# Kernel optimization log

Measured on AMD Instinct MI355X. Metric: run time of the kernel, lower is better.

The kernel has to match this reference:

```python
import jax, jax.numpy as jnp
import numpy as np

N_NODES = 30000
N_EDGES = 480000
IN = 64
HID = 32
OUT = 64
H1, H2 = 4, 4


def _xavier(key, shape, gain=1.4142135623730951):
    fan_out, fan_in = shape
    std = gain * (2.0 / (fan_in + fan_out)) ** 0.5
    return std * jax.random.normal(key, shape, dtype=jnp.float32)


def setup_inputs() -> dict:
    key = jax.random.key(0)
    ks = jax.random.split(key, 12)
    nfeats = jax.random.normal(ks[0], (N_NODES, IN), dtype=jnp.float32)
    efeats = jax.random.normal(ks[1], (N_EDGES, IN), dtype=jnp.float32)
    src = jax.random.randint(ks[2], (N_EDGES,), 0, N_NODES, dtype=jnp.int32)
    dst = jax.random.randint(ks[3], (N_EDGES,), 0, N_NODES, dtype=jnp.int32)
    # layer 1 params: in_node=IN, in_edge=IN, out_node=out_edge=HID, heads=H1
    W_nodes1 = _xavier(ks[4], (HID * H1, IN))
    b_nodes1 = jnp.zeros((HID * H1,), dtype=jnp.float32)
    W_edges1 = _xavier(ks[5], (HID * H1, 3 * IN))
    W_attn1 = _xavier(ks[6], (H1, HID))
    # layer 2 params: in_node=in_edge=HID*H1, out_node=out_edge=OUT, heads=H2
    d2 = HID * H1
    W_nodes2 = _xavier(ks[7], (OUT * H2, d2))
    b_nodes2 = jnp.zeros((OUT * H2,), dtype=jnp.float32)
    W_edges2 = _xavier(ks[8], (OUT * H2, 3 * d2))
    W_attn2 = _xavier(ks[9], (H2, OUT))
    return {
        "nfeats": nfeats, "efeats": efeats, "src": src, "dst": dst,
        "W_nodes1": W_nodes1, "b_nodes1": b_nodes1, "W_edges1": W_edges1, "W_attn1": W_attn1,
        "W_nodes2": W_nodes2, "b_nodes2": b_nodes2, "W_edges2": W_edges2, "W_attn2": W_attn2,
    }


def _egat_layer(hn, he, src, dst, Wn, bn, We, Wa, num_heads, out_n, out_e, first_layer, n_nodes):
    # first layer: node 'h' overwritten by sum-aggregation of incoming edge feats
    if first_layer:
        hn = jax.ops.segment_sum(he, dst, num_segments=n_nodes)
    E = he.shape[0]
    # edge attention on raw node feats: [h_src | f | h_dst] -> fc_edges -> leaky_relu
    stack = jnp.concatenate([hn[src], he, hn[dst]], axis=-1)          # [E, 2*dn + de]
    f_out = jax.nn.leaky_relu(stack @ We.T)                            # [E, H*out_e]
    f_out = f_out.reshape(E, num_heads, out_e)                         # new edge feats
    # a = fc_attn(f_out).sum(-1)  ==  f_out . (column-sum of W_attn)
    a = jnp.einsum("ehf,f->eh", f_out, Wa.sum(axis=0))                 # [E, H]
    # projected node feats used as messages
    hp = (hn @ Wn.T + bn).reshape(n_nodes, num_heads, out_n)           # [N, H, out_n]
    # segment softmax of a over edges sharing the same dst
    amax = jax.ops.segment_max(a, dst, num_segments=n_nodes)
    amax = jnp.where(jnp.isfinite(amax), amax, 0.0)
    ex = jnp.exp(a - amax[dst])
    den = jax.ops.segment_sum(ex, dst, num_segments=n_nodes)
    alpha = ex / jnp.maximum(den[dst], 1e-9)                           # [E, H]
    # weighted scatter-sum of src messages into dst nodes
    h_out = jax.ops.segment_sum(alpha[..., None] * hp[src], dst, num_segments=n_nodes)
    return h_out, f_out


def reference(nfeats, efeats, src, dst,
              W_nodes1, b_nodes1, W_edges1, W_attn1,
              W_nodes2, b_nodes2, W_edges2, W_attn2):
    n_nodes = nfeats.shape[0]
    # layer 1 (first_layer=True, activation=elu), then flatten heads
    hn, he = _egat_layer(nfeats, efeats, src, dst, W_nodes1, b_nodes1, W_edges1,
                         W_attn1, H1, HID, HID, True, n_nodes)
    hn = jax.nn.elu(hn).reshape(n_nodes, H1 * HID)
    he = jax.nn.elu(he).reshape(-1, H1 * HID)
    # layer 2 (no activation), then mean over heads
    hn, he = _egat_layer(hn, he, src, dst, W_nodes2, b_nodes2, W_edges2,
                         W_attn2, H2, OUT, OUT, False, n_nodes)
    hn = hn.mean(axis=1)
    he = he.mean(axis=1)
    return hn, he
```

## Files before the change

kernel.cpp:

```cpp
#include <hip/hip_runtime.h>
#include <hip/hip_fp16.h>
#include <math.h>

#define NN 30000
#define NE 480000

typedef short bf16x8 __attribute__((ext_vector_type(8)));
typedef float f32x4 __attribute__((ext_vector_type(4)));

static __device__ __forceinline__ unsigned short f2b(float f) {
    union { float f; unsigned u; } v; v.f = f;
    unsigned r = v.u + 0x7FFF + ((v.u >> 16) & 1);
    return (unsigned short)(r >> 16);
}
static __device__ __forceinline__ float b2f(unsigned short s) {
    union { unsigned u; float f; } v; v.u = ((unsigned)s) << 16; return v.f;
}
static __device__ __forceinline__ unsigned short f2h(float f) {
    return __half_as_ushort(__float2half(f));
}
static __device__ __forceinline__ float2 uph2(unsigned u) {
    __half2 h = *(__half2*)&u;
    float2 r; r.x = __low2float(h); r.y = __high2float(h); return r;
}

static __device__ __forceinline__ float rowsum16(float v) {
    union { float f; int i; } u, t;
    u.f = v;
    t.i = __builtin_amdgcn_update_dpp(0, u.i, 0x111, 0xf, 0xf, true); u.f += t.f;
    t.i = __builtin_amdgcn_update_dpp(0, u.i, 0x112, 0xf, 0xf, true); u.f += t.f;
    t.i = __builtin_amdgcn_update_dpp(0, u.i, 0x114, 0xf, 0xf, true); u.f += t.f;
    t.i = __builtin_amdgcn_update_dpp(0, u.i, 0x118, 0xf, 0xf, true); u.f += t.f;
    return u.f;
}

__global__ void k_count(const int* __restrict__ dst, int* __restrict__ cnt) {
    int e = blockIdx.x * 256 + threadIdx.x;
    if (e < NE) atomicAdd(&cnt[dst[e]], 1);
}

__global__ __launch_bounds__(1024) void k_scanA(const int* __restrict__ cnt,
                                                int* __restrict__ off,
                                                int* __restrict__ bsum) {
    __shared__ int s[1024];
    int tid = threadIdx.x;
    int i = blockIdx.x * 1024 + tid;
    int v = (i < NN) ? cnt[i] : 0;
    s[tid] = v;
    __syncthreads();
    for (int d = 1; d < 1024; d <<= 1) {
        int t = (tid >= d) ? s[tid - d] : 0;
        __syncthreads();
        s[tid] += t;
        __syncthreads();
    }
    if (i < NN) off[i] = s[tid] - v;
    if (tid == 1023) bsum[blockIdx.x] = s[1023];
}

__global__ void k_scanB(const int* __restrict__ bsum, int* __restrict__ bbase, int nb) {
    if (threadIdx.x == 0) {
        int run = 0;
        for (int i = 0; i < nb; ++i) { bbase[i] = run; run += bsum[i]; }
    }
}

__global__ __launch_bounds__(1024) void k_scanC(int* __restrict__ off,
                                                int* __restrict__ cur,
                                                const int* __restrict__ bbase) {
    int i = blockIdx.x * 1024 + threadIdx.x;
    if (i < NN) {
        int o = off[i] + bbase[blockIdx.x];
        off[i] = o;
        cur[i] = o;
        if (i == 0) off[NN] = NE;
    }
}

__global__ void k_fill(const int* __restrict__ dst, int* __restrict__ cur,
                       int* __restrict__ eid) {
    int e = blockIdx.x * 256 + threadIdx.x;
    if (e < NE) {
        int p = atomicAdd(&cur[dst[e]], 1);
        eid[p] = e;
    }
}

__global__ void k_perm(const float* __restrict__ ef, const int* __restrict__ eid,
                       const int* __restrict__ src, const int* __restrict__ dst,
                       unsigned short* __restrict__ efb_p, int* __restrict__ src_p,
                       int* __restrict__ dst_p) {
    int gid = blockIdx.x * 256 + threadIdx.x;
    if (gid >= NE * 8) return;
    int i = gid >> 3, sub = gid & 7;
    int e = eid[i];
    if (sub == 0) { src_p[i] = src[e]; dst_p[i] = dst[e]; }
    const float4* p = (const float4*)(ef + (size_t)e * 64 + sub * 8);
    float4 x = p[0], y = p[1];
    uint4 o;
    o.x = (unsigned)f2b(x.x) | ((unsigned)f2b(x.y) << 16);
    o.y = (unsigned)f2b(x.z) | ((unsigned)f2b(x.w) << 16);
    o.z = (unsigned)f2b(y.x) | ((unsigned)f2b(y.y) << 16);
    o.w = (unsigned)f2b(y.z) | ((unsigned)f2b(y.w) << 16);
    *(uint4*)(efb_p + (size_t)i * 64 + sub * 8) = o;
}

__global__ void k_convw(const float* __restrict__ We1, const float* __restrict__ We2,
                        unsigned short* __restrict__ W1b, unsigned short* __restrict__ W2b) {
    int i = blockIdx.x * 256 + threadIdx.x;
    if (i < 128 * 64) {
        int r = i >> 6, k = i & 63;
        W1b[i] = f2b(We1[(size_t)r * 192 + 64 + k]);
    } else if (i < 128 * 64 + 256 * 128) {
        int j = i - 128 * 64;
        int r = j >> 7, k = j & 127;
        W2b[j] = f2b(We2[(size_t)r * 384 + 128 + k]);
    }
}

__global__ void k_convsplit(const float* __restrict__ Wn1, const float* __restrict__ We1,
                            const float* __restrict__ Wn2, const float* __restrict__ We2,
                            unsigned short* __restrict__ W1h, unsigned short* __restrict__ W1l,
                            unsigned short* __restrict__ W2h, unsigned short* __restrict__ W2l) {
    int i = blockIdx.x * 256 + threadIdx.x;
    if (i < 384 * 64) {
        int r = i >> 6, k = i & 63;
        float v;
        if (r < 128)      v = Wn1[(size_t)r * 64 + k];
        else if (r < 256) v = We1[(size_t)(r - 128) * 192 + k];
        else              v = We1[(size_t)(r - 256) * 192 + 128 + k];
        unsigned short h = f2b(v);
        W1h[i] = h; W1l[i] = f2b(v - b2f(h));
    } else if (i < 384 * 64 + 768 * 128) {
        int j = i - 384 * 64;
        int r = j >> 7, k = j & 127;
        float v;
        if (r < 256)      v = Wn2[(size_t)r * 128 + k];
        else if (r < 512) v = We2[(size_t)(r - 256) * 384 + k];
        else              v = We2[(size_t)(r - 512) * 384 + 256 + k];
        unsigned short h = f2b(v);
        W2h[j] = h; W2l[j] = f2b(v - b2f(h));
    }
}

__global__ void k_agg_ef(const float* __restrict__ ef, const int* __restrict__ off,
                         const int* __restrict__ eid,
                         unsigned short* __restrict__ hn1h, unsigned short* __restrict__ hn1l) {
    int w = (blockIdx.x * 256 + threadIdx.x) >> 6;
    int lane = threadIdx.x & 63;
    if (w >= NN) return;
    int s0 = off[w], s1 = off[w + 1];
    float acc = 0.f;
    int i = s0;
    for (; i + 2 <= s1; i += 2) {
        int e0 = eid[i], e1 = eid[i + 1];
        float v0 = ef[(size_t)e0 * 64 + lane];
        float v1 = ef[(size_t)e1 * 64 + lane];
        acc += v0;
        acc += v1;
    }
    for (; i < s1; ++i) {
        int e = eid[i];
        acc += ef[(size_t)e * 64 + lane];
    }
    unsigned short h = f2b(acc);
    hn1h[(size_t)w * 64 + lane] = h;
    hn1l[(size_t)w * 64 + lane] = f2b(acc - b2f(h));
}

static __device__ __forceinline__ void store_p1(unsigned short* hp1, unsigned short* pa1,
                                                unsigned short* pc1, int n, int o, float v) {
    unsigned short h = f2h(v);
    if (o < 128) {
        hp1[(size_t)n * 128 + (o & 63) * 2 + (o >> 6)] = h;
    } else if (o < 256) {
        int x = o - 128;
        pa1[(size_t)n * 128 + ((x >> 5) * 16 + (x & 15)) * 2 + ((x >> 4) & 1)] = h;
    } else {
        int x = o - 256;
        pc1[(size_t)n * 128 + ((x >> 5) * 16 + (x & 15)) * 2 + ((x >> 4) & 1)] = h;
    }
}

static __device__ __forceinline__ void store_p2(unsigned short* hp2, unsigned short* pa2,
                                                unsigned short* pc2, int n, int o, float v) {
    unsigned short h = f2h(v);
    if (o < 256) {
        hp2[(size_t)n * 256 + (o & 63) * 4 + (o >> 6)] = h;
    } else if (o < 512) {
        int x = o - 256;
        pa2[(size_t)n * 256 + (x & 63) * 4 + (x >> 6)] = h;
    } else {
        int x = o - 512;
        pc2[(size_t)n * 256 + (x & 63) * 4 + (x >> 6)] = h;
    }
}

__global__ __launch_bounds__(256) void k_nodeproj1(
        const unsigned short* __restrict__ hn1h, const unsigned short* __restrict__ hn1l,
        const unsigned short* __restrict__ W1h, const unsigned short* __restrict__ W1l,
        const float* __restrict__ b1,
        unsigned short* __restrict__ hp1, unsigned short* __restrict__ pa1,
        unsigned short* __restrict__ pc1) {
    int tid = threadIdx.x;
    int w = tid >> 6, l = tid & 63;
    int c = l & 15, g = l >> 4;
    int pb = blockIdx.x * 16;

    f32x4 acc[6];
#pragma unroll
    for (int t = 0; t < 6; ++t) acc[t] = (f32x4)(0.f);

#pragma unroll
    for (int kk = 0; kk < 2; ++kk) {
        int arow = pb + c;
        bf16x8 ah = *(const bf16x8*)&hn1h[(size_t)arow * 64 + kk * 32 + g * 8];
        bf16x8 al = *(const bf16x8*)&hn1l[(size_t)arow * 64 + kk * 32 + g * 8];
#pragma unroll
        for (int t = 0; t < 6; ++t) {
            int brow = w * 96 + t * 16 + c;
            bf16x8 bh = *(const bf16x8*)&W1h[(size_t)brow * 64 + kk * 32 + g * 8];
            bf16x8 bl = *(const bf16x8*)&W1l[(size_t)brow * 64 + kk * 32 + g * 8];
            acc[t] = __builtin_amdgcn_mfma_f32_16x16x32_bf16(ah, bh, acc[t], 0, 0, 0);
            acc[t] = __builtin_amdgcn_mfma_f32_16x16x32_bf16(ah, bl, acc[t], 0, 0, 0);
            acc[t] = __builtin_amdgcn_mfma_f32_16x16x32_bf16(al, bh, acc[t], 0, 0, 0);
        }
    }

#pragma unroll
    for (int t = 0; t < 6; ++t) {
        int og = w * 96 + t * 16 + c;
        float bias = (og < 128) ? b1[og] : 0.f;
#pragma unroll
        for (int r = 0; r < 4; ++r) {
            int n = pb + g * 4 + r;
            if (n < NN) store_p1(hp1, pa1, pc1, n, og, acc[t][r] + bias);
        }
    }
}

__global__ __launch_bounds__(256) void k_gemm1(
        const unsigned short* __restrict__ efb_p, const int* __restrict__ src_p,
        const int* __restrict__ dst_p, const unsigned short* __restrict__ W1b,
        const float* __restrict__ Wa1, const unsigned short* __restrict__ pa1,
        const unsigned short* __restrict__ pc1,
        unsigned short* __restrict__ he1b, float* __restrict__ a1) {
    int tid = threadIdx.x;
    int w = tid >> 6, l = tid & 63;
    int c = l & 15, g = l >> 4;
    int pb = blockIdx.x * 64;

    f32x4 acc[4][2];
    for (int m = 0; m < 4; ++m)
        for (int t = 0; t < 2; ++t) acc[m][t] = (f32x4)(0.f);

#pragma unroll
    for (int kk = 0; kk < 2; ++kk) {
        bf16x8 b[2];
#pragma unroll
        for (int t = 0; t < 2; ++t)
            b[t] = *(const bf16x8*)&W1b[(size_t)((2 * w + t) * 16 + c) * 64 + kk * 32 + g * 8];
#pragma unroll
        for (int m = 0; m < 4; ++m) {
            bf16x8 a = *(const bf16x8*)&efb_p[(size_t)(pb + m * 16 + c) * 64 + kk * 32 + g * 8];
#pragma unroll
            for (int t = 0; t < 2; ++t)
                acc[m][t] = __builtin_amdgcn_mfma_f32_16x16x32_bf16(a, b[t], acc[m][t], 0, 0, 0);
        }
    }

    float wsj0 = Wa1[c] + Wa1[32 + c] + Wa1[64 + c] + Wa1[96 + c];
    float wsj1 = Wa1[16 + c] + Wa1[48 + c] + Wa1[80 + c] + Wa1[112 + c];
    const unsigned* paH = (const unsigned*)pa1;
    const unsigned* pcH = (const unsigned*)pc1;

    int ss[16], dd[16];
#pragma unroll
    for (int m = 0; m < 4; ++m) {
        int4 s4 = *(const int4*)&src_p[pb + m * 16 + g * 4];
        int4 d4 = *(const int4*)&dst_p[pb + m * 16 + g * 4];
        ss[m * 4 + 0] = s4.x; ss[m * 4 + 1] = s4.y; ss[m * 4 + 2] = s4.z; ss[m * 4 + 3] = s4.w;
        dd[m * 4 + 0] = d4.x; dd[m * 4 + 1] = d4.y; dd[m * 4 + 2] = d4.z; dd[m * 4 + 3] = d4.w;
    }

#pragma unroll
    for (int m = 0; m < 4; ++m) {
        unsigned ua[4], uc[4];
#pragma unroll
        for (int r = 0; r < 4; ++r) {
            ua[r] = paH[(size_t)ss[m * 4 + r] * 64 + w * 16 + c];
            uc[r] = pcH[(size_t)dd[m * 4 + r] * 64 + w * 16 + c];
        }
#pragma unroll
        for (int r = 0; r < 4; ++r) {
            int pos = pb + m * 16 + g * 4 + r;
            float2 av2 = uph2(ua[r]);
            float2 cv2 = uph2(uc[r]);
            float f0 = acc[m][0][r] + av2.x + cv2.x;
            float f1 = acc[m][1][r] + av2.y + cv2.y;
            float lf0 = (f0 > 0.f) ? f0 : 0.01f * f0;
            float lf1 = (f1 > 0.f) ? f1 : 0.01f * f1;
            float av = lf0 * wsj0 + lf1 * wsj1;
            he1b[(size_t)pos * 128 + w * 32 + c]      = f2b((lf0 > 0.f) ? lf0 : expm1f(lf0));
            he1b[(size_t)pos * 128 + w * 32 + 16 + c] = f2b((lf1 > 0.f) ? lf1 : expm1f(lf1));
            av = rowsum16(av);
            if (c == 15) a1[(size_t)pos * 4 + w] = av;
        }
    }
}

__global__ void k_agg1(const float* __restrict__ a1, const int* __restrict__ off,
                       const int* __restrict__ src_p, const unsigned short* __restrict__ hp1,
                       unsigned short* __restrict__ hn1oh, unsigned short* __restrict__ hn1ol) {
    __shared__ float4 alf[4][64];
    int wv = threadIdx.x >> 6;
    int w = (blockIdx.x * 256 + threadIdx.x) >> 6;
    int lane = threadIdx.x & 63;
    if (w >= NN) return;
    int s0 = off[w], s1 = off[w + 1];
    if (s1 == s0) {
        hn1oh[(size_t)w * 128 + lane] = 0; hn1oh[(size_t)w * 128 + 64 + lane] = 0;
        hn1ol[(size_t)w * 128 + lane] = 0; hn1ol[(size_t)w * 128 + 64 + lane] = 0;
        return;
    }
    float m[4] = {-INFINITY, -INFINITY, -INFINITY, -INFINITY};
    for (int i = s0 + lane; i < s1; i += 64) {
        float4 av = *(const float4*)&a1[(size_t)i * 4];
        m[0] = fmaxf(m[0], av.x); m[1] = fmaxf(m[1], av.y);
        m[2] = fmaxf(m[2], av.z); m[3] = fmaxf(m[3], av.w);
    }
#pragma unroll
    for (int d = 1; d < 64; d <<= 1) {
        m[0] = fmaxf(m[0], __shfl_xor(m[0], d, 64));
        m[1] = fmaxf(m[1], __shfl_xor(m[1], d, 64));
        m[2] = fmaxf(m[2], __shfl_xor(m[2], d, 64));
        m[3] = fmaxf(m[3], __shfl_xor(m[3], d, 64));
    }
    float den[4] = {0.f, 0.f, 0.f, 0.f};
    for (int i = s0 + lane; i < s1; i += 64) {
        float4 av = *(const float4*)&a1[(size_t)i * 4];
        den[0] += expf(av.x - m[0]); den[1] += expf(av.y - m[1]);
        den[2] += expf(av.z - m[2]); den[3] += expf(av.w - m[3]);
    }
#pragma unroll
    for (int d = 1; d < 64; d <<= 1) {
        den[0] += __shfl_xor(den[0], d, 64);
        den[1] += __shfl_xor(den[1], d, 64);
        den[2] += __shfl_xor(den[2], d, 64);
        den[3] += __shfl_xor(den[3], d, 64);
    }
    float r0 = 1.f / den[0], r1 = 1.f / den[1], r2 = 1.f / den[2], r3 = 1.f / den[3];
    int h0 = lane >> 5;
    const unsigned* hpH = (const unsigned*)hp1;
    float acc0 = 0.f, acc1 = 0.f;
    for (int base = s0; base < s1; base += 64) {
        int i = base + lane;
        if (i < s1) {
            float4 av = *(const float4*)&a1[(size_t)i * 4];
            float4 al;
            al.x = expf(av.x - m[0]) * r0;
            al.y = expf(av.y - m[1]) * r1;
            al.z = expf(av.z - m[2]) * r2;
            al.w = expf(av.w - m[3]) * r3;
            alf[wv][lane] = al;
        }
        int lim = s1 - base; if (lim > 64) lim = 64;
        int k = 0;
        for (; k + 8 <= lim; k += 8) {
            int sx[8];
            unsigned ux[8];
#pragma unroll
            for (int q = 0; q < 8; ++q) sx[q] = src_p[base + k + q];
#pragma unroll
            for (int q = 0; q < 8; ++q) ux[q] = hpH[(size_t)sx[q] * 64 + lane];
#pragma unroll
            for (int q = 0; q < 8; ++q) {
                float4 aq = alf[wv][k + q];
                float2 u = uph2(ux[q]);
                float w0 = (h0 == 0) ? aq.x : aq.y;
                float w1 = (h0 == 0) ? aq.z : aq.w;
                acc0 += w0 * u.x;
                acc1 += w1 * u.y;
            }
        }
        for (; k < lim; ++k) {
            float4 al = alf[wv][k];
            int s = src_p[base + k];
            float2 u = uph2(hpH[(size_t)s * 64 + lane]);
            float w0 = (h0 == 0) ? al.x : al.y;
            float w1 = (h0 == 0) ? al.z : al.w;
            acc0 += w0 * u.x;
            acc1 += w1 * u.y;
        }
    }
    float e0 = (acc0 > 0.f) ? acc0 : expm1f(acc0);
    float e1 = (acc1 > 0.f) ? acc1 : expm1f(acc1);
    unsigned short h0s = f2b(e0), h1s = f2b(e1);
    hn1oh[(size_t)w * 128 + lane] = h0s;
    hn1ol[(size_t)w * 128 + lane] = f2b(e0 - b2f(h0s));
    hn1oh[(size_t)w * 128 + 64 + lane] = h1s;
    hn1ol[(size_t)w * 128 + 64 + lane] = f2b(e1 - b2f(h1s));
}

__global__ __launch_bounds__(256) void k_nodeproj2(
        const unsigned short* __restrict__ hn1oh, const unsigned short* __restrict__ hn1ol,
        const unsigned short* __restrict__ W2h, const unsigned short* __restrict__ W2l,
        const float* __restrict__ b2,
        unsigned short* __restrict__ hp2, unsigned short* __restrict__ pa2,
        unsigned short* __restrict__ pc2) {
    int tid = threadIdx.x;
    int w = tid >> 6, l = tid & 63;
    int c = l & 15, g = l >> 4;
    int pb = blockIdx.x * 16;

    f32x4 acc[12];
#pragma unroll
    for (int t = 0; t < 12; ++t) acc[t] = (f32x4)(0.f);

#pragma unroll
    for (int kk = 0; kk < 4; ++kk) {
        int arow = pb + c;
        bf16x8 ah = *(const bf16x8*)&hn1oh[(size_t)arow * 128 + kk * 32 + g * 8];
        bf16x8 al = *(const bf16x8*)&hn1ol[(size_t)arow * 128 + kk * 32 + g * 8];
#pragma unroll
        for (int t = 0; t < 12; ++t) {
            int brow = w * 192 + t * 16 + c;
            bf16x8 bh = *(const bf16x8*)&W2h[(size_t)brow * 128 + kk * 32 + g * 8];
            bf16x8 bl = *(const bf16x8*)&W2l[(size_t)brow * 128 + kk * 32 + g * 8];
            acc[t] = __builtin_amdgcn_mfma_f32_16x16x32_bf16(ah, bh, acc[t], 0, 0, 0);
            acc[t] = __builtin_amdgcn_mfma_f32_16x16x32_bf16(ah, bl, acc[t], 0, 0, 0);
            acc[t] = __builtin_amdgcn_mfma_f32_16x16x32_bf16(al, bh, acc[t], 0, 0, 0);
        }
    }

#pragma unroll
    for (int t = 0; t < 12; ++t) {
        int og = w * 192 + t * 16 + c;
        float bias = (og < 256) ? b2[og] : 0.f;
#pragma unroll
        for (int r = 0; r < 4; ++r) {
            int n = pb + g * 4 + r;
            if (n < NN) store_p2(hp2, pa2, pc2, n, og, acc[t][r] + bias);
        }
    }
}

__global__ __launch_bounds__(256) void k_gemm2(
        const unsigned short* __restrict__ he1b, const int* __restrict__ src_p,
        const int* __restrict__ dst_p, const int* __restrict__ eid,
        const unsigned short* __restrict__ W2b, const float* __restrict__ Wa2,
        const unsigned short* __restrict__ pa2, const unsigned short* __restrict__ pc2,
        float* __restrict__ heo, float* __restrict__ a2) {
    __shared__ float a2l[4 * 64 * 4];
    int tid = threadIdx.x;
    int w = tid >> 6, l = tid & 63;
    int c = l & 15, g = l >> 4;
    int j = w * 16 + c;
    int pb = blockIdx.x * 64;

    f32x4 acc[4][4];
    for (int m = 0; m < 4; ++m)
        for (int t = 0; t < 4; ++t) acc[m][t] = (f32x4)(0.f);

#pragma unroll
    for (int kk = 0; kk < 4; ++kk) {
        bf16x8 b[4];
#pragma unroll
        for (int t = 0; t < 4; ++t)
            b[t] = *(const bf16x8*)&W2b[(size_t)((w + 4 * t) * 16 + c) * 128 + kk * 32 + g * 8];
#pragma unroll
        for (int m = 0; m < 4; ++m) {
            bf16x8 a = *(const bf16x8*)&he1b[(size_t)(pb + m * 16 + c) * 128 + kk * 32 + g * 8];
#pragma unroll
            for (int t = 0; t < 4; ++t)
                acc[m][t] = __builtin_amdgcn_mfma_f32_16x16x32_bf16(a, b[t], acc[m][t], 0, 0, 0);
        }
    }

    float wsj = Wa2[j] + Wa2[64 + j] + Wa2[128 + j] + Wa2[192 + j];
    const uint2* paH = (const uint2*)pa2;
    const uint2* pcH = (const uint2*)pc2;

    int ss[16], dd[16];
#pragma unroll
    for (int m = 0; m < 4; ++m) {
        int4 s4 = *(const int4*)&src_p[pb + m * 16 + g * 4];
        int4 d4 = *(const int4*)&dst_p[pb + m * 16 + g * 4];
        ss[m * 4 + 0] = s4.x; ss[m * 4 + 1] = s4.y; ss[m * 4 + 2] = s4.z; ss[m * 4 + 3] = s4.w;
        dd[m * 4 + 0] = d4.x; dd[m * 4 + 1] = d4.y; dd[m * 4 + 2] = d4.z; dd[m * 4 + 3] = d4.w;
    }

#pragma unroll
    for (int m = 0; m < 4; ++m) {
        uint2 ua[4], uc[4];
#pragma unroll
        for (int r = 0; r < 4; ++r) {
            ua[r] = paH[(size_t)ss[m * 4 + r] * 64 + j];
            uc[r] = pcH[(size_t)dd[m * 4 + r] * 64 + j];
        }
        int4 e4 = *(const int4*)&eid[pb + m * 16 + g * 4];
        int ee[4] = {e4.x, e4.y, e4.z, e4.w};
#pragma unroll
        for (int r = 0; r < 4; ++r) {
            int le = m * 16 + g * 4 + r;
            float2 a01 = uph2(ua[r].x), a23 = uph2(ua[r].y);
            float2 c01 = uph2(uc[r].x), c23 = uph2(uc[r].y);
            float f[4];
            f[0] = acc[m][0][r] + a01.x + c01.x;
            f[1] = acc[m][1][r] + a01.y + c01.y;
            f[2] = acc[m][2][r] + a23.x + c23.x;
            f[3] = acc[m][3][r] + a23.y + c23.y;
            float hsum = 0.f;
            float avt[4];
#pragma unroll
            for (int t = 0; t < 4; ++t) {
                float lf = (f[t] > 0.f) ? f[t] : 0.01f * f[t];
                hsum += lf;
                avt[t] = lf * wsj;
            }
#pragma unroll
            for (int t = 0; t < 4; ++t) avt[t] = rowsum16(avt[t]);
            if (c == 15) {
                float4 st = make_float4(avt[0], avt[1], avt[2], avt[3]);
                *(float4*)&a2l[(w * 64 + le) * 4] = st;
            }
            heo[(size_t)ee[r] * 64 + j] = 0.25f * hsum;
        }
    }
    __syncthreads();
    {
        int pos = tid >> 2, t = tid & 3;
        float v = a2l[(0 * 64 + pos) * 4 + t] + a2l[(1 * 64 + pos) * 4 + t]
                + a2l[(2 * 64 + pos) * 4 + t] + a2l[(3 * 64 + pos) * 4 + t];
        a2[(size_t)(pb + pos) * 4 + t] = v;
    }
}

__global__ void k_agg2(const float* __restrict__ a2, const int* __restrict__ off,
                       const int* __restrict__ src_p, const unsigned short* __restrict__ hp2,
                       float* __restrict__ hno) {
    __shared__ float4 alf[4][64];
    int wv = threadIdx.x >> 6;
    int w = (blockIdx.x * 256 + threadIdx.x) >> 6;
    int lane = threadIdx.x & 63;
    if (w >= NN) return;
    int s0 = off[w], s1 = off[w + 1];
    if (s1 == s0) {
        hno[(size_t)w * 64 + lane] = 0.f;
        return;
    }
    float m[4] = {-INFINITY, -INFINITY, -INFINITY, -INFINITY};
    for (int i = s0 + lane; i < s1; i += 64) {
        float4 av = *(const float4*)&a2[(size_t)i * 4];
        m[0] = fmaxf(m[0], av.x); m[1] = fmaxf(m[1], av.y);
        m[2] = fmaxf(m[2], av.z); m[3] = fmaxf(m[3], av.w);
    }
#pragma unroll
    for (int d = 1; d < 64; d <<= 1) {
        m[0] = fmaxf(m[0], __shfl_xor(m[0], d, 64));
        m[1] = fmaxf(m[1], __shfl_xor(m[1], d, 64));
        m[2] = fmaxf(m[2], __shfl_xor(m[2], d, 64));
        m[3] = fmaxf(m[3], __shfl_xor(m[3], d, 64));
    }
    float den[4] = {0.f, 0.f, 0.f, 0.f};
    for (int i = s0 + lane; i < s1; i += 64) {
        float4 av = *(const float4*)&a2[(size_t)i * 4];
        den[0] += expf(av.x - m[0]); den[1] += expf(av.y - m[1]);
        den[2] += expf(av.z - m[2]); den[3] += expf(av.w - m[3]);
    }
#pragma unroll
    for (int d = 1; d < 64; d <<= 1) {
        den[0] += __shfl_xor(den[0], d, 64);
        den[1] += __shfl_xor(den[1], d, 64);
        den[2] += __shfl_xor(den[2], d, 64);
        den[3] += __shfl_xor(den[3], d, 64);
    }
    float r0 = 1.f / den[0], r1 = 1.f / den[1], r2 = 1.f / den[2], r3 = 1.f / den[3];
    const uint2* hpH = (const uint2*)hp2;
    float acc0 = 0.f, acc1 = 0.f, acc2 = 0.f, acc3 = 0.f;
    for (int base = s0; base < s1; base += 64) {
        int i = base + lane;
        if (i < s1) {
            float4 av = *(const float4*)&a2[(size_t)i * 4];
            float4 al;
            al.x = expf(av.x - m[0]) * r0;
            al.y = expf(av.y - m[1]) * r1;
            al.z = expf(av.z - m[2]) * r2;
            al.w = expf(av.w - m[3]) * r3;
            alf[wv][lane] = al;
        }
        int lim = s1 - base; if (lim > 64) lim = 64;
        int k = 0;
        for (; k + 8 <= lim; k += 8) {
            int sx[8];
            uint2 ux[8];
#pragma unroll
            for (int q = 0; q < 8; ++q) sx[q] = src_p[base + k + q];
#pragma unroll
            for (int q = 0; q < 8; ++q) ux[q] = hpH[(size_t)sx[q] * 64 + lane];
#pragma unroll
            for (int q = 0; q < 8; ++q) {
                float4 aq = alf[wv][k + q];
                float2 u01 = uph2(ux[q].x), u23 = uph2(ux[q].y);
                acc0 += aq.x * u01.x;
                acc1 += aq.y * u01.y;
                acc2 += aq.z * u23.x;
                acc3 += aq.w * u23.y;
            }
        }
        for (; k < lim; ++k) {
            float4 al = alf[wv][k];
            int s = src_p[base + k];
            uint2 u = hpH[(size_t)s * 64 + lane];
            float2 u01 = uph2(u.x), u23 = uph2(u.y);
            acc0 += al.x * u01.x;
            acc1 += al.y * u01.y;
            acc2 += al.z * u23.x;
            acc3 += al.w * u23.y;
        }
    }
    hno[(size_t)w * 64 + lane] = 0.25f * (acc0 + acc1 + acc2 + acc3);
}

extern "C" void kernel_launch(void* const* d_in, const int* in_sizes, int n_in,
                              void* d_out, int out_size, void* d_ws, size_t ws_size,
                              hipStream_t stream) {
    const float* efeats = (const float*)d_in[1];
    const int* src = (const int*)d_in[2];
    const int* dst = (const int*)d_in[3];
    const float* Wn1 = (const float*)d_in[4];
    const float* b1  = (const float*)d_in[5];
    const float* We1 = (const float*)d_in[6];
    const float* Wa1 = (const float*)d_in[7];
    const float* Wn2 = (const float*)d_in[8];
    const float* b2  = (const float*)d_in[9];
    const float* We2 = (const float*)d_in[10];
    const float* Wa2 = (const float*)d_in[11];

    const int NNP = 30016;

    char* ws = (char*)d_ws;
    size_t o = 0;
    auto alloc = [&](size_t bytes) {
        void* p = ws + o;
        o += (bytes + 255) & ~(size_t)255;
        return p;
    };
    int* cnt   = (int*)alloc((size_t)NN * 4);
    int* off   = (int*)alloc((size_t)(NN + 1) * 4);
    int* cur   = (int*)alloc((size_t)NN * 4);
    int* eid   = (int*)alloc((size_t)NE * 4);
    int* src_p = (int*)alloc((size_t)NE * 4);
    int* dst_p = (int*)alloc((size_t)NE * 4);
    int* bsum  = (int*)alloc(64 * 4);
    int* bbase = (int*)alloc(64 * 4);
    float* a1  = (float*)alloc((size_t)NE * 4 * 4);
    unsigned short* efb_p = (unsigned short*)alloc((size_t)NE * 64 * 2);
    unsigned short* he1b  = (unsigned short*)alloc((size_t)NE * 128 * 2);
    unsigned short* W1b   = (unsigned short*)alloc((size_t)128 * 64 * 2);
    unsigned short* W2b   = (unsigned short*)alloc((size_t)256 * 128 * 2);
    unsigned short* W1h   = (unsigned short*)alloc((size_t)384 * 64 * 2);
    unsigned short* W1l   = (unsigned short*)alloc((size_t)384 * 64 * 2);
    unsigned short* W2h   = (unsigned short*)alloc((size_t)768 * 128 * 2);
    unsigned short* W2l   = (unsigned short*)alloc((size_t)768 * 128 * 2);
    unsigned short* hn1h  = (unsigned short*)alloc((size_t)NNP * 64 * 2);
    unsigned short* hn1l  = (unsigned short*)alloc((size_t)NNP * 64 * 2);
    unsigned short* hn1oh = (unsigned short*)alloc((size_t)NNP * 128 * 2);
    unsigned short* hn1ol = (unsigned short*)alloc((size_t)NNP * 128 * 2);
    unsigned short* hp1   = (unsigned short*)alloc((size_t)NN * 128 * 2);
    unsigned short* pa1   = (unsigned short*)alloc((size_t)NN * 128 * 2);
    unsigned short* pc1   = (unsigned short*)alloc((size_t)NN * 128 * 2);
    unsigned short* hp2   = (unsigned short*)alloc((size_t)NN * 256 * 2);
    unsigned short* pa2   = (unsigned short*)alloc((size_t)NN * 256 * 2);
    unsigned short* pc2   = (unsigned short*)alloc((size_t)NN * 256 * 2);

    float* hno = (float*)d_out;
    float* heo = (float*)d_out + (size_t)NN * 64;

    const int SCAN_B = (NN + 1023) / 1024;
    const int NPB = NNP / 16;
    hipMemsetAsync(cnt, 0, (size_t)NN * 4, stream);
    k_count<<<(NE + 255) / 256, 256, 0, stream>>>(dst, cnt);
    k_scanA<<<SCAN_B, 1024, 0, stream>>>(cnt, off, bsum);
    k_scanB<<<1, 64, 0, stream>>>(bsum, bbase, SCAN_B);
    k_scanC<<<SCAN_B, 1024, 0, stream>>>(off, cur, bbase);
    k_fill<<<(NE + 255) / 256, 256, 0, stream>>>(dst, cur, eid);
    k_convw<<<(128 * 64 + 256 * 128 + 255) / 256, 256, 0, stream>>>(We1, We2, W1b, W2b);
    k_convsplit<<<(384 * 64 + 768 * 128 + 255) / 256, 256, 0, stream>>>(
        Wn1, We1, Wn2, We2, W1h, W1l, W2h, W2l);
    k_perm<<<NE * 8 / 256, 256, 0, stream>>>(efeats, eid, src, dst, efb_p, src_p, dst_p);
    k_agg_ef<<<NN / 4, 256, 0, stream>>>(efeats, off, eid, hn1h, hn1l);
    k_nodeproj1<<<NPB, 256, 0, stream>>>(hn1h, hn1l, W1h, W1l, b1, hp1, pa1, pc1);
    k_gemm1<<<NE / 64, 256, 0, stream>>>(efb_p, src_p, dst_p, W1b, Wa1, pa1, pc1, he1b, a1);
    k_agg1<<<NN / 4, 256, 0, stream>>>(a1, off, src_p, hp1, hn1oh, hn1ol);
    k_nodeproj2<<<NPB, 256, 0, stream>>>(hn1oh, hn1ol, W2h, W2l, b2, hp2, pa2, pc2);
    k_gemm2<<<NE / 64, 256, 0, stream>>>(he1b, src_p, dst_p, eid, W2b, Wa2, pa2, pc2, heo, a1);
    k_agg2<<<NN / 4, 256, 0, stream>>>(a1, off, src_p, hp2, hno);
}
```

Before: 686.8 us.

## Fuse edge permutation into edge-feature aggregation and prefetch gathers in GEMMs

```diff
diff --git a/kernel.cpp b/kernel.cpp
--- a/kernel.cpp
+++ b/kernel.cpp
@@ -84,25 +84,6 @@
         int p = atomicAdd(&cur[dst[e]], 1);
         eid[p] = e;
     }
-}
-
-__global__ void k_perm(const float* __restrict__ ef, const int* __restrict__ eid,
-                       const int* __restrict__ src, const int* __restrict__ dst,
-                       unsigned short* __restrict__ efb_p, int* __restrict__ src_p,
-                       int* __restrict__ dst_p) {
-    int gid = blockIdx.x * 256 + threadIdx.x;
-    if (gid >= NE * 8) return;
-    int i = gid >> 3, sub = gid & 7;
-    int e = eid[i];
-    if (sub == 0) { src_p[i] = src[e]; dst_p[i] = dst[e]; }
-    const float4* p = (const float4*)(ef + (size_t)e * 64 + sub * 8);
-    float4 x = p[0], y = p[1];
-    uint4 o;
-    o.x = (unsigned)f2b(x.x) | ((unsigned)f2b(x.y) << 16);
-    o.y = (unsigned)f2b(x.z) | ((unsigned)f2b(x.w) << 16);
-    o.z = (unsigned)f2b(y.x) | ((unsigned)f2b(y.y) << 16);
-    o.w = (unsigned)f2b(y.z) | ((unsigned)f2b(y.w) << 16);
-    *(uint4*)(efb_p + (size_t)i * 64 + sub * 8) = o;
 }
 
 __global__ void k_convw(const float* __restrict__ We1, const float* __restrict__ We2,
@@ -143,25 +124,42 @@
     }
 }
 
-__global__ void k_agg_ef(const float* __restrict__ ef, const int* __restrict__ off,
-                         const int* __restrict__ eid,
-                         unsigned short* __restrict__ hn1h, unsigned short* __restrict__ hn1l) {
+__global__ void k_permagg(const float* __restrict__ ef, const int* __restrict__ eid,
+                          const int* __restrict__ src, const int* __restrict__ dst,
+                          const int* __restrict__ off,
+                          unsigned short* __restrict__ efb_p, int* __restrict__ src_p,
+                          int* __restrict__ dst_p,
+                          unsigned short* __restrict__ hn1h, unsigned short* __restrict__ hn1l) {
     int w = (blockIdx.x * 256 + threadIdx.x) >> 6;
     int lane = threadIdx.x & 63;
     if (w >= NN) return;
     int s0 = off[w], s1 = off[w + 1];
     float acc = 0.f;
     int i = s0;
-    for (; i + 2 <= s1; i += 2) {
-        int e0 = eid[i], e1 = eid[i + 1];
+    for (; i + 4 <= s1; i += 4) {
+        int e0 = eid[i], e1 = eid[i + 1], e2 = eid[i + 2], e3 = eid[i + 3];
         float v0 = ef[(size_t)e0 * 64 + lane];
         float v1 = ef[(size_t)e1 * 64 + lane];
-        acc += v0;
-        acc += v1;
+        float v2 = ef[(size_t)e2 * 64 + lane];
+        float v3 = ef[(size_t)e3 * 64 + lane];
+        if (lane == 0) {
+            src_p[i] = src[e0]; dst_p[i] = dst[e0];
+            src_p[i + 1] = src[e1]; dst_p[i + 1] = dst[e1];
+            src_p[i + 2] = src[e2]; dst_p[i + 2] = dst[e2];
+            src_p[i + 3] = src[e3]; dst_p[i + 3] = dst[e3];
+        }
+        efb_p[(size_t)i * 64 + lane] = f2b(v0);
+        efb_p[(size_t)(i + 1) * 64 + lane] = f2b(v1);
+        efb_p[(size_t)(i + 2) * 64 + lane] = f2b(v2);
+        efb_p[(size_t)(i + 3) * 64 + lane] = f2b(v3);
+        acc += v0; acc += v1; acc += v2; acc += v3;
     }
     for (; i < s1; ++i) {
         int e = eid[i];
-        acc += ef[(size_t)e * 64 + lane];
+        float v = ef[(size_t)e * 64 + lane];
+        if (lane == 0) { src_p[i] = src[e]; dst_p[i] = dst[e]; }
+        efb_p[(size_t)i * 64 + lane] = f2b(v);
+        acc += v;
     }
     unsigned short h = f2b(acc);
     hn1h[(size_t)w * 64 + lane] = h;
@@ -283,19 +281,27 @@
         dd[m * 4 + 0] = d4.x; dd[m * 4 + 1] = d4.y; dd[m * 4 + 2] = d4.z; dd[m * 4 + 3] = d4.w;
     }
 
+    unsigned ua[2][4], uc[2][4];
+#pragma unroll
+    for (int r = 0; r < 4; ++r) {
+        ua[0][r] = paH[(size_t)ss[r] * 64 + w * 16 + c];
+        uc[0][r] = pcH[(size_t)dd[r] * 64 + w * 16 + c];
+    }
+
 #pragma unroll
     for (int m = 0; m < 4; ++m) {
-        unsigned ua[4], uc[4];
-#pragma unroll
-        for (int r = 0; r < 4; ++r) {
-            ua[r] = paH[(size_t)ss[m * 4 + r] * 64 + w * 16 + c];
-            uc[r] = pcH[(size_t)dd[m * 4 + r] * 64 + w * 16 + c];
+        if (m < 3) {
+#pragma unroll
+            for (int r = 0; r < 4; ++r) {
+                ua[(m + 1) & 1][r] = paH[(size_t)ss[(m + 1) * 4 + r] * 64 + w * 16 + c];
+                uc[(m + 1) & 1][r] = pcH[(size_t)dd[(m + 1) * 4 + r] * 64 + w * 16 + c];
+            }
         }
 #pragma unroll
         for (int r = 0; r < 4; ++r) {
             int pos = pb + m * 16 + g * 4 + r;
-            float2 av2 = uph2(ua[r]);
-            float2 cv2 = uph2(uc[r]);
+            float2 av2 = uph2(ua[m & 1][r]);
+            float2 cv2 = uph2(uc[m & 1][r]);
             float f0 = acc[m][0][r] + av2.x + cv2.x;
             float f1 = acc[m][1][r] + av2.y + cv2.y;
             float lf0 = (f0 > 0.f) ? f0 : 0.01f * f0;
@@ -490,21 +496,29 @@
         dd[m * 4 + 0] = d4.x; dd[m * 4 + 1] = d4.y; dd[m * 4 + 2] = d4.z; dd[m * 4 + 3] = d4.w;
     }
 
+    uint2 ua[2][4], uc[2][4];
+#pragma unroll
+    for (int r = 0; r < 4; ++r) {
+        ua[0][r] = paH[(size_t)ss[r] * 64 + j];
+        uc[0][r] = pcH[(size_t)dd[r] * 64 + j];
+    }
+
 #pragma unroll
     for (int m = 0; m < 4; ++m) {
-        uint2 ua[4], uc[4];
-#pragma unroll
-        for (int r = 0; r < 4; ++r) {
-            ua[r] = paH[(size_t)ss[m * 4 + r] * 64 + j];
-            uc[r] = pcH[(size_t)dd[m * 4 + r] * 64 + j];
+        if (m < 3) {
+#pragma unroll
+            for (int r = 0; r < 4; ++r) {
+                ua[(m + 1) & 1][r] = paH[(size_t)ss[(m + 1) * 4 + r] * 64 + j];
+                uc[(m + 1) & 1][r] = pcH[(size_t)dd[(m + 1) * 4 + r] * 64 + j];
+            }
         }
         int4 e4 = *(const int4*)&eid[pb + m * 16 + g * 4];
         int ee[4] = {e4.x, e4.y, e4.z, e4.w};
 #pragma unroll
         for (int r = 0; r < 4; ++r) {
             int le = m * 16 + g * 4 + r;
-            float2 a01 = uph2(ua[r].x), a23 = uph2(ua[r].y);
-            float2 c01 = uph2(uc[r].x), c23 = uph2(uc[r].y);
+            float2 a01 = uph2(ua[m & 1][r].x), a23 = uph2(ua[m & 1][r].y);
+            float2 c01 = uph2(uc[m & 1][r].x), c23 = uph2(uc[m & 1][r].y);
             float f[4];
             f[0] = acc[m][0][r] + a01.x + c01.x;
             f[1] = acc[m][1][r] + a01.y + c01.y;
@@ -688,8 +702,8 @@
     k_convw<<<(128 * 64 + 256 * 128 + 255) / 256, 256, 0, stream>>>(We1, We2, W1b, W2b);
     k_convsplit<<<(384 * 64 + 768 * 128 + 255) / 256, 256, 0, stream>>>(
         Wn1, We1, Wn2, We2, W1h, W1l, W2h, W2l);
-    k_perm<<<NE * 8 / 256, 256, 0, stream>>>(efeats, eid, src, dst, efb_p, src_p, dst_p);
-    k_agg_ef<<<NN / 4, 256, 0, stream>>>(efeats, off, eid, hn1h, hn1l);
+    k_permagg<<<NN / 4, 256, 0, stream>>>(efeats, eid, src, dst, off, efb_p, src_p, dst_p,
+                                          hn1h, hn1l);
     k_nodeproj1<<<NPB, 256, 0, stream>>>(hn1h, hn1l, W1h, W1l, b1, hp1, pa1, pc1);
     k_gemm1<<<NE / 64, 256, 0, stream>>>(efb_p, src_p, dst_p, W1b, Wa1, pa1, pc1, he1b, a1);
     k_agg1<<<NN / 4, 256, 0, stream>>>(a1, off, src_p, hp1, hn1oh, hn1ol);
```

Result: faster. 672.3 us (-2.1%).
